# Performance work log

Measured on AMD Instinct MI355X. Metric: run time of the kernel, lower is better.

## Reference

```python
import jax, jax.numpy as jnp
import numpy as np

B, CIN, COUT, K, SDIM, H, W = 8, 512, 256, 3, 512, 64, 64


def _blur_kernel():
    k = jnp.array([1.0, 3.0, 3.0, 1.0], dtype=jnp.float32)
    k = k[None, :] * k[:, None]
    k = k / k.sum()
    return k * 4.0  # upsample_factor ** 2


def setup_inputs() -> dict:
    key = jax.random.key(0)
    ks = jax.random.split(key, 4)
    return {
        "x": jax.random.normal(ks[0], (B, CIN, H, W), jnp.float32),
        "style": jax.random.normal(ks[1], (B, SDIM), jnp.float32),
        "weight": jax.random.normal(ks[2], (1, COUT, CIN, K, K), jnp.float32),
        "mod_weight": jax.random.normal(ks[3], (CIN, SDIM), jnp.float32),
        "mod_bias": jnp.ones((CIN,), jnp.float32),
    }


def reference(x, style, weight, mod_weight, mod_bias):
    b, cin, h, w = x.shape
    cout = weight.shape[1]
    k = weight.shape[-1]
    scale = 1.0 / np.sqrt(cin * k * k)          # fan_in of conv weight
    mod_scale = 1.0 / np.sqrt(mod_weight.shape[1])  # EqualLinear scale

    # modulation: EqualLinear(style) -> [B, Cin]
    s = style @ (mod_weight * mod_scale).T + mod_bias

    # per-sample modulated + demodulated weight [B, Cout, Cin, K, K]
    wmod = scale * weight * s[:, None, :, None, None]
    demod = jax.lax.rsqrt(jnp.sum(wmod * wmod, axis=(2, 3, 4)) + 1e-8)
    wmod = wmod * demod[:, :, None, None, None]

    # conv_transpose2d(stride=2, padding=0) == dilated conv with lhs_dilation=2,
    # padding K-1 on each side, spatially flipped kernel. Output (H-1)*2 + K.
    wflip = jnp.flip(wmod, axis=(-2, -1))

    def per_sample(xi, wi):
        return jax.lax.conv_general_dilated(
            xi[None], wi, window_strides=(1, 1),
            padding=[(k - 1, k - 1)] * 2, lhs_dilation=(2, 2),
            dimension_numbers=("NCHW", "OIHW", "NCHW"))[0]

    out = jax.vmap(per_sample)(x, wflip)  # [B, Cout, 2H+1, 2W+1] for K=3

    # Blur (upfirdn2d, up=1): torch does conv2d with flip(kernel);
    # lax conv is also correlation, so use flipped kernel, depthwise.
    bk = jnp.flip(_blur_kernel(), (0, 1))
    p = 4 - 2 - (k - 1)
    pad0 = (p + 1) // 2 + 1
    pad1 = p // 2 + 1
    wblur = jnp.broadcast_to(bk[None, None], (cout, 1, 4, 4))
    out = jax.lax.conv_general_dilated(
        out, wblur, (1, 1), [(pad0, pad1), (pad0, pad1)],
        feature_group_count=cout,
        dimension_numbers=("NCHW", "OIHW", "NCHW"))
    return out  # [B, Cout, 2H, 2W]
```

## Files before the change

### kernel.cpp

```cpp
#include <hip/hip_runtime.h>
#include <hip/hip_bf16.h>
#include <stdint.h>

typedef unsigned short u16;
typedef __attribute__((ext_vector_type(8))) short short8;
typedef __attribute__((ext_vector_type(4))) float floatx4;

__device__ __forceinline__ u16 f2bf(float f) {
    union { unsigned int i; float f; } v; v.f = f;
    unsigned int r = v.i + 0x7fff + ((v.i >> 16) & 1);
    return (u16)(r >> 16);
}

#define OFF_S    0
#define OFF_DEM  16384
#define OFF_W2   32768
#define OFF_BM   1048576
#define OFF_XMT  16777216

__global__ void k_style(const float* __restrict__ style, const float* __restrict__ mw,
                        const float* __restrict__ mb, float* __restrict__ S) {
    int t = blockIdx.x * 256 + threadIdx.x;
    int b = t >> 9, ci = t & 511;
    const float* sr = style + b * 512;
    const float* wr = mw + ci * 512;
    float acc = 0.f;
    for (int d = 0; d < 512; d += 4) {
        float4 sv = *(const float4*)(sr + d);
        float4 wv = *(const float4*)(wr + d);
        acc += sv.x * wv.x + sv.y * wv.y + sv.z * wv.z + sv.w * wv.w;
    }
    S[t] = acc * 0.044194173824159216f + mb[ci];
}

__global__ void k_w2(const float* __restrict__ w, float* __restrict__ W2) {
    int t = blockIdx.x * 256 + threadIdx.x;
    const float* p = w + t * 9;
    float a = 0.f;
    #pragma unroll
    for (int i = 0; i < 9; ++i) { float v = p[i]; a += v * v; }
    W2[t] = a;
}

__global__ void k_demod(const float* __restrict__ W2, const float* __restrict__ S,
                        float* __restrict__ D) {
    int t = blockIdx.x * 256 + threadIdx.x;
    int b = t >> 8, co = t & 255;
    const float* wr = W2 + co * 512;
    const float* sr = S + b * 512;
    float a = 0.f;
    for (int ci = 0; ci < 512; ++ci) { float s = sr[ci]; a += wr[ci] * s * s; }
    D[t] = 0.014731391274719738f * rsqrtf(a * (1.0f / 4608.0f) + 1e-8f);
}

__global__ void k_bmat(const float* __restrict__ Wt, u16* __restrict__ Bm) {
    int t = blockIdx.x * 256 + threadIdx.x;
    int ci = t & 511;
    int rest = t >> 9;
    int co = rest & 255;
    int p = rest >> 8;
    int py = p >> 1, px = p & 1;
    const float KT[2][3][3] = {
        {{0.f,1.f,3.f},{3.f,3.f,1.f},{1.f,0.f,0.f}},
        {{0.f,0.f,1.f},{1.f,3.f,3.f},{3.f,1.f,0.f}}
    };
    float wv[3][3];
    const float* wp = Wt + (co * 512 + ci) * 9;
    #pragma unroll
    for (int a = 0; a < 3; ++a)
        #pragma unroll
        for (int bq = 0; bq < 3; ++bq) wv[a][bq] = wp[a * 3 + bq];
    int n = py * 512 + co * 2 + px;
    size_t base = (size_t)n * 4608 + ci;
    #pragma unroll
    for (int dyi = 0; dyi < 3; ++dyi) {
        #pragma unroll
        for (int dxi = 0; dxi < 3; ++dxi) {
            float val = 0.f;
            #pragma unroll
            for (int a = 0; a < 3; ++a) {
                float ky = KT[py][dyi][a];
                #pragma unroll
                for (int bq = 0; bq < 3; ++bq)
                    val += wv[a][bq] * (ky * KT[px][dxi][bq]);
            }
            Bm[base + (dyi * 3 + dxi) * 512] = f2bf(val * 0.0625f);
        }
    }
}

__global__ void k_zero(u16* __restrict__ XMT) {
    size_t t = (size_t)blockIdx.x * 256 + threadIdx.x;
    *(short8*)(XMT + t * 8) = (short8)0;
}

__global__ void k_fill(const float* __restrict__ X, const float* __restrict__ S,
                       u16* __restrict__ XMT) {
    __shared__ __align__(16) u16 tile[64][80];
    int blk = blockIdx.x;
    int ci0g = (blk & 7) * 64;
    int h = (blk >> 3) & 63;
    int b = blk >> 9;
    int t = threadIdx.x;
    #pragma unroll
    for (int it = 0; it < 4; ++it) {
        int idx = it * 256 + t;
        int ci_l = idx >> 4, ch = idx & 15;
        float4 v = *(const float4*)(X + (((b * 512 + ci0g + ci_l) * 64 + h) * 64 + ch * 4));
        float s = S[b * 512 + ci0g + ci_l];
        tile[ch * 4 + 0][ci_l] = f2bf(v.x * s);
        tile[ch * 4 + 1][ci_l] = f2bf(v.y * s);
        tile[ch * 4 + 2][ci_l] = f2bf(v.z * s);
        tile[ch * 4 + 3][ci_l] = f2bf(v.w * s);
    }
    __syncthreads();
    #pragma unroll
    for (int it = 0; it < 2; ++it) {
        int idx = it * 256 + t;
        int wl = idx >> 3, c8 = idx & 7;
        short8 v = *(const short8*)(&tile[wl][c8 * 8]);
        *(short8*)(XMT + (((size_t)(b * 66 + h + 1) * 66 + (wl + 1)) * 512 + ci0g + c8 * 8)) = v;
    }
}


#define GLDS(SRC, DST) __builtin_amdgcn_global_load_lds( \
    (const __attribute__((address_space(1))) void*)(SRC), \
    (__attribute__((address_space(3))) void*)(DST), 16, 0, 0)

#define BAR() do { asm volatile("" ::: "memory"); \
                   __builtin_amdgcn_s_barrier(); \
                   asm volatile("" ::: "memory"); } while (0)

#define WAITV(n) asm volatile("s_waitcnt vmcnt(" #n ")" ::: "memory")

#define STAGE_A(d, h, kt) do { int _o = offA(kt); \
    GLDS(X  + preA[h][0] + _o, smem + (d)*32768 + (h)*16384 + t*16); \
    GLDS(X  + preA[h][1] + _o, smem + (d)*32768 + (h)*16384 + 8192 + t*16); \
  } while (0)
#define STAGE_B(d, h, kt) do { int _o = (kt)*64; \
    GLDS(Bm + preB[h][0] + _o, smem + 65536 + (d)*32768 + (h)*16384 + t*16); \
    GLDS(Bm + preB[h][1] + _o, smem + 65536 + (d)*32768 + (h)*16384 + 8192 + t*16); \
  } while (0)

#define LOAD_A(d, mh) do { \
    _Pragma("unroll") \
    for (int mt_ = 0; mt_ < 4; ++mt_) { \
      afr[mt_][0] = *(const short8*)(smem + (d)*32768 + (mh)*16384 + mt_*2048 + baseMA + cb0); \
      afr[mt_][1] = *(const short8*)(smem + (d)*32768 + (mh)*16384 + mt_*2048 + baseMA + cb1); \
    } } while (0)
#define LOAD_B(d, nh, DST) do { \
    _Pragma("unroll") \
    for (int nt_ = 0; nt_ < 2; ++nt_) { \
      DST[nt_][0] = *(const short8*)(smem + 65536 + (d)*32768 + (nh)*16384 + nt_*2048 + baseNB + cb0); \
      DST[nt_][1] = *(const short8*)(smem + 65536 + (d)*32768 + (nh)*16384 + nt_*2048 + baseNB + cb1); \
    } } while (0)

#define MMA(mh, nh, BF) do { \
    __builtin_amdgcn_s_setprio(1); \
    _Pragma("unroll") \
    for (int mt_ = 0; mt_ < 4; ++mt_) \
      _Pragma("unroll") \
      for (int nt_ = 0; nt_ < 2; ++nt_) { \
        acc[mh][mt_][nh][nt_] = __builtin_amdgcn_mfma_f32_16x16x32_bf16( \
            afr[mt_][0], BF[nt_][0], acc[mh][mt_][nh][nt_], 0, 0, 0); \
        acc[mh][mt_][nh][nt_] = __builtin_amdgcn_mfma_f32_16x16x32_bf16( \
            afr[mt_][1], BF[nt_][1], acc[mh][mt_][nh][nt_], 0, 0, 0); \
      } \
    __builtin_amdgcn_s_setprio(0); \
  } while (0)

__global__ __launch_bounds__(512, 2)
void k_main8(const u16* __restrict__ X, const u16* __restrict__ Bm,
             const float* __restrict__ D, float* __restrict__ out) {
    __shared__ __align__(16) char smem[131072];
    const int t = threadIdx.x;
    const int swz = (blockIdx.x & 7) * 64 + (blockIdx.x >> 3);
    const int bn = swz & 3, bm = swz >> 2;
    const int w = t >> 6, L = t & 63;
    const int wm = w >> 2, wn = w & 3;
    const int quad = L >> 4, col = L & 15;

    int preA[2][2], preB[2][2];
    #pragma unroll
    for (int h = 0; h < 2; ++h)
      #pragma unroll
      for (int i = 0; i < 2; ++i) {
        int sig = i * 512 + t;
        int ml = sig >> 3;
        int ks = (sig & 7) ^ (ml & 7);
        int mg = bm * 256 + h * 128 + ml;
        int b_ = mg >> 12, r = (mg >> 6) & 63, c = mg & 63;
        preA[h][i] = ((b_ * 66 + r) * 66 + c) * 512 + ks * 8;
        int ng = bn * 256 + h * 128 + ml;
        preB[h][i] = ng * 4608 + ks * 8;
      }
    auto offA = [](int kt) {
        int j = kt >> 3;
        int dy = (j * 11) >> 5;
        int dx = j - dy * 3;
        return (dy * 66 + dx) * 512 + (kt & 7) * 64;
    };

    const int baseMA = (wm * 64 + col) * 128;
    const int baseNB = (wn * 32 + col) * 128;
    const int cb0 = ((0 * 4 + quad) ^ (col & 7)) * 16;
    const int cb1 = ((1 * 4 + quad) ^ (col & 7)) * 16;

    short8 afr[4][2], bf0[2][2], bf1[2][2];
    floatx4 acc[2][4][2][2];
    #pragma unroll
    for (int mh = 0; mh < 2; ++mh)
      #pragma unroll
      for (int mt = 0; mt < 4; ++mt)
        #pragma unroll
        for (int nh = 0; nh < 2; ++nh)
          #pragma unroll
          for (int nt = 0; nt < 2; ++nt)
            acc[mh][mt][nh][nt] = (floatx4){0.f, 0.f, 0.f, 0.f};

    STAGE_A(0, 0, 0); STAGE_B(0, 0, 0);
    STAGE_A(0, 1, 0); STAGE_B(0, 1, 0);
    STAGE_A(1, 0, 1); STAGE_B(1, 0, 1);
    WAITV(4);
    BAR();

    #pragma unroll 1
    for (int it = 0; it < 35; ++it) {
        const int k = 2 * it;
        LOAD_A(0, 0); LOAD_B(0, 0, bf0);
        STAGE_A(1, 1, k + 1);
        BAR(); MMA(0, 0, bf0); BAR();
        LOAD_B(0, 1, bf1);
        STAGE_B(1, 1, k + 1);
        BAR(); MMA(0, 1, bf1); BAR();
        LOAD_A(0, 1);
        STAGE_A(0, 0, k + 2);
        BAR(); MMA(1, 0, bf0); BAR();
        STAGE_B(0, 0, k + 2);
        WAITV(4);
        BAR(); MMA(1, 1, bf1); BAR();
        LOAD_A(1, 0); LOAD_B(1, 0, bf0);
        STAGE_A(0, 1, k + 2);
        BAR(); MMA(0, 0, bf0); BAR();
        LOAD_B(1, 1, bf1);
        STAGE_B(0, 1, k + 2);
        BAR(); MMA(0, 1, bf1); BAR();
        LOAD_A(1, 1);
        STAGE_A(1, 0, k + 3);
        BAR(); MMA(1, 0, bf0); BAR();
        STAGE_B(1, 0, k + 3);
        WAITV(4);
        BAR(); MMA(1, 1, bf1); BAR();
    }

    LOAD_A(0, 0); LOAD_B(0, 0, bf0);
    STAGE_A(1, 1, 71);
    BAR(); MMA(0, 0, bf0); BAR();
    LOAD_B(0, 1, bf1);
    STAGE_B(1, 1, 71);
    BAR(); MMA(0, 1, bf1); BAR();
    LOAD_A(0, 1);
    BAR(); MMA(1, 0, bf0); BAR();
    WAITV(0);
    BAR(); MMA(1, 1, bf1); BAR();
    LOAD_A(1, 0); LOAD_B(1, 0, bf0);
    BAR(); MMA(0, 0, bf0); BAR();
    LOAD_B(1, 1, bf1);
    BAR(); MMA(0, 1, bf1); BAR();
    LOAD_A(1, 1);
    BAR(); MMA(1, 0, bf0); BAR();
    BAR(); MMA(1, 1, bf1); BAR();

    const int b   = bm >> 4;
    const int r0  = (bm & 15) * 4;
    const int py  = bn >> 1;
    const int co0 = (bn & 1) * 128;
    float dvals[2][2];
    #pragma unroll
    for (int nh = 0; nh < 2; ++nh)
      #pragma unroll
      for (int nt = 0; nt < 2; ++nt)
        dvals[nh][nt] = D[b * 256 + co0 + nh * 64 + wn * 16 + nt * 8 + (col >> 1)];

    float* ep = (float*)smem;
    #pragma unroll
    for (int rl = 0; rl < 4; ++rl) {
        if (wm == (rl & 1)) {
            const int mh = rl >> 1;
            #pragma unroll
            for (int nh = 0; nh < 2; ++nh)
              #pragma unroll
              for (int nt = 0; nt < 2; ++nt) {
                float dsv = dvals[nh][nt];
                int coL = nh * 64 + wn * 16 + nt * 8 + (col >> 1);
                #pragma unroll
                for (int mt = 0; mt < 4; ++mt)
                  #pragma unroll
                  for (int reg = 0; reg < 4; ++reg) {
                    int x = 2 * (mt * 16 + quad * 4 + reg) + (col & 1);
                    ep[coL * 132 + x] = acc[mh][mt][nh][nt][reg] * dsv;
                  }
              }
        }
        __syncthreads();
        #pragma unroll
        for (int itc = 0; itc < 8; ++itc) {
            int s = itc * 512 + t;
            int co = s >> 5, xi = s & 31;
            float4 v = *(const float4*)(ep + co * 132 + xi * 4);
            size_t o = ((size_t)((b * 256 + co0 + co) * 128 + (2 * (r0 + rl) + py))) * 128 + xi * 4;
            *(float4*)(out + o) = v;
        }
        __syncthreads();
    }
}

extern "C" void kernel_launch(void* const* d_in, const int* in_sizes, int n_in,
                              void* d_out, int out_size, void* d_ws, size_t ws_size,
                              hipStream_t stream) {
    const float* x      = (const float*)d_in[0];
    const float* style  = (const float*)d_in[1];
    const float* weight = (const float*)d_in[2];
    const float* mw     = (const float*)d_in[3];
    const float* mb     = (const float*)d_in[4];
    float* out = (float*)d_out;
    char* ws = (char*)d_ws;
    float* S   = (float*)(ws + OFF_S);
    float* DEM = (float*)(ws + OFF_DEM);
    float* W2  = (float*)(ws + OFF_W2);
    u16*  BM   = (u16*)(ws + OFF_BM);
    u16*  XMT  = (u16*)(ws + OFF_XMT);

    k_style<<<16,   256, 0, stream>>>(style, mw, mb, S);
    k_w2   <<<512,  256, 0, stream>>>(weight, W2);
    k_demod<<<8,    256, 0, stream>>>(W2, S, DEM);
    k_bmat <<<2048, 256, 0, stream>>>(weight, BM);
    k_zero <<<8712, 256, 0, stream>>>(XMT);
    k_fill <<<4096, 256, 0, stream>>>(x, S, XMT);
    k_main8<<<512,  512, 0, stream>>>(XMT, BM, DEM, out);
}
```

Before: 476.7 us.

## Parallelize prologue kernels, fold border zeroing into fill, swizzle fill LDS

The style and demodulation reductions now give each output one wavefront and reduce with shuffles, so they launch many more blocks instead of a handful of serial-loop threads. The weight-to-B-matrix kernel stages each block's weights through shared memory so the strided 9-float reads become coalesced. The separate zeroing pass over the padded activation buffer is removed and only the one-pixel halo is zeroed inside the fill kernel. The fill kernel's transpose tile gets an XOR swizzle to cut LDS bank conflicts. The risk is that halo zeroing is now spread across fill blocks, and correctness depends on every border cell being covered.

Measured after the change: 428.4 us. 1.11x faster.

```diff
diff --git a/kernel.cpp b/kernel.cpp
--- a/kernel.cpp
+++ b/kernel.cpp
@@ -20,17 +20,20 @@
 
 __global__ void k_style(const float* __restrict__ style, const float* __restrict__ mw,
                         const float* __restrict__ mb, float* __restrict__ S) {
-    int t = blockIdx.x * 256 + threadIdx.x;
-    int b = t >> 9, ci = t & 511;
-    const float* sr = style + b * 512;
-    const float* wr = mw + ci * 512;
-    float acc = 0.f;
-    for (int d = 0; d < 512; d += 4) {
-        float4 sv = *(const float4*)(sr + d);
-        float4 wv = *(const float4*)(wr + d);
-        acc += sv.x * wv.x + sv.y * wv.y + sv.z * wv.z + sv.w * wv.w;
-    }
-    S[t] = acc * 0.044194173824159216f + mb[ci];
+    int g = blockIdx.x * 4 + (threadIdx.x >> 6);
+    int lane = threadIdx.x & 63;
+    int b = g >> 9, ci = g & 511;
+    const float* sr = style + b * 512 + lane * 8;
+    const float* wr = mw + ci * 512 + lane * 8;
+    float4 s0 = *(const float4*)(sr);
+    float4 s1 = *(const float4*)(sr + 4);
+    float4 w0 = *(const float4*)(wr);
+    float4 w1 = *(const float4*)(wr + 4);
+    float acc = s0.x * w0.x + s0.y * w0.y + s0.z * w0.z + s0.w * w0.w
+              + s1.x * w1.x + s1.y * w1.y + s1.z * w1.z + s1.w * w1.w;
+    #pragma unroll
+    for (int o = 32; o; o >>= 1) acc += __shfl_xor(acc, o, 64);
+    if (lane == 0) S[g] = acc * 0.044194173824159216f + mb[ci];
 }
 
 __global__ void k_w2(const float* __restrict__ w, float* __restrict__ W2) {
@@ -44,32 +47,44 @@
 
 __global__ void k_demod(const float* __restrict__ W2, const float* __restrict__ S,
                         float* __restrict__ D) {
-    int t = blockIdx.x * 256 + threadIdx.x;
-    int b = t >> 8, co = t & 255;
-    const float* wr = W2 + co * 512;
-    const float* sr = S + b * 512;
-    float a = 0.f;
-    for (int ci = 0; ci < 512; ++ci) { float s = sr[ci]; a += wr[ci] * s * s; }
-    D[t] = 0.014731391274719738f * rsqrtf(a * (1.0f / 4608.0f) + 1e-8f);
+    int g = blockIdx.x * 4 + (threadIdx.x >> 6);
+    int lane = threadIdx.x & 63;
+    int b = g >> 8, co = g & 255;
+    const float* wr = W2 + co * 512 + lane * 8;
+    const float* sr = S + b * 512 + lane * 8;
+    float4 w0 = *(const float4*)(wr);
+    float4 w1 = *(const float4*)(wr + 4);
+    float4 s0 = *(const float4*)(sr);
+    float4 s1 = *(const float4*)(sr + 4);
+    float a = w0.x * s0.x * s0.x + w0.y * s0.y * s0.y + w0.z * s0.z * s0.z + w0.w * s0.w * s0.w
+            + w1.x * s1.x * s1.x + w1.y * s1.y * s1.y + w1.z * s1.z * s1.z + w1.w * s1.w * s1.w;
+    #pragma unroll
+    for (int o = 32; o; o >>= 1) a += __shfl_xor(a, o, 64);
+    if (lane == 0) D[g] = 0.014731391274719738f * rsqrtf(a * (1.0f / 4608.0f) + 1e-8f);
 }
 
 __global__ void k_bmat(const float* __restrict__ Wt, u16* __restrict__ Bm) {
-    int t = blockIdx.x * 256 + threadIdx.x;
-    int ci = t & 511;
-    int rest = t >> 9;
-    int co = rest & 255;
-    int p = rest >> 8;
+    __shared__ float wl[2304];
+    int blk = blockIdx.x;
+    int tid = threadIdx.x;
+    int ci0 = (blk & 1) * 256;
+    int co  = (blk >> 1) & 255;
+    int p   = blk >> 9;
     int py = p >> 1, px = p & 1;
+    int wbase = co * 4608 + ci0 * 9;
+    #pragma unroll
+    for (int j = 0; j < 9; ++j) wl[j * 256 + tid] = Wt[wbase + j * 256 + tid];
+    __syncthreads();
     const float KT[2][3][3] = {
         {{0.f,1.f,3.f},{3.f,3.f,1.f},{1.f,0.f,0.f}},
         {{0.f,0.f,1.f},{1.f,3.f,3.f},{3.f,1.f,0.f}}
     };
     float wv[3][3];
-    const float* wp = Wt + (co * 512 + ci) * 9;
     #pragma unroll
     for (int a = 0; a < 3; ++a)
         #pragma unroll
-        for (int bq = 0; bq < 3; ++bq) wv[a][bq] = wp[a * 3 + bq];
+        for (int bq = 0; bq < 3; ++bq) wv[a][bq] = wl[tid * 9 + a * 3 + bq];
+    int ci = ci0 + tid;
     int n = py * 512 + co * 2 + px;
     size_t base = (size_t)n * 4608 + ci;
     #pragma unroll
@@ -89,11 +104,6 @@
     }
 }
 
-__global__ void k_zero(u16* __restrict__ XMT) {
-    size_t t = (size_t)blockIdx.x * 256 + threadIdx.x;
-    *(short8*)(XMT + t * 8) = (short8)0;
-}
-
 __global__ void k_fill(const float* __restrict__ X, const float* __restrict__ S,
                        u16* __restrict__ XMT) {
     __shared__ __align__(16) u16 tile[64][80];
@@ -102,23 +112,36 @@
     int h = (blk >> 3) & 63;
     int b = blk >> 9;
     int t = threadIdx.x;
+    if (t < 16) {
+        int x = (t >> 3) ? 65 : 0;
+        int c8 = t & 7;
+        *(short8*)(XMT + ((size_t)(b * 66 + h + 1) * 66 + x) * 512 + ci0g + c8 * 8) = (short8)0;
+    }
+    if (h == 0 || h == 63) {
+        int y = (h == 0) ? 0 : 65;
+        for (int s0 = t; s0 < 528; s0 += 256) {
+            int x = s0 >> 3, c8 = s0 & 7;
+            *(short8*)(XMT + ((size_t)(b * 66 + y) * 66 + x) * 512 + ci0g + c8 * 8) = (short8)0;
+        }
+    }
     #pragma unroll
     for (int it = 0; it < 4; ++it) {
         int idx = it * 256 + t;
         int ci_l = idx >> 4, ch = idx & 15;
         float4 v = *(const float4*)(X + (((b * 512 + ci0g + ci_l) * 64 + h) * 64 + ch * 4));
         float s = S[b * 512 + ci0g + ci_l];
-        tile[ch * 4 + 0][ci_l] = f2bf(v.x * s);
-        tile[ch * 4 + 1][ci_l] = f2bf(v.y * s);
-        tile[ch * 4 + 2][ci_l] = f2bf(v.z * s);
-        tile[ch * 4 + 3][ci_l] = f2bf(v.w * s);
+        int cisw = ci_l ^ ((ch & 7) << 3);
+        tile[ch * 4 + 0][cisw] = f2bf(v.x * s);
+        tile[ch * 4 + 1][cisw] = f2bf(v.y * s);
+        tile[ch * 4 + 2][cisw] = f2bf(v.z * s);
+        tile[ch * 4 + 3][cisw] = f2bf(v.w * s);
     }
     __syncthreads();
     #pragma unroll
     for (int it = 0; it < 2; ++it) {
         int idx = it * 256 + t;
         int wl = idx >> 3, c8 = idx & 7;
-        short8 v = *(const short8*)(&tile[wl][c8 * 8]);
+        short8 v = *(const short8*)(&tile[wl][(c8 ^ ((wl >> 2) & 7)) * 8]);
         *(short8*)(XMT + (((size_t)(b * 66 + h + 1) * 66 + (wl + 1)) * 512 + ci0g + c8 * 8)) = v;
     }
 }
@@ -332,11 +355,10 @@
     u16*  BM   = (u16*)(ws + OFF_BM);
     u16*  XMT  = (u16*)(ws + OFF_XMT);
 
-    k_style<<<16,   256, 0, stream>>>(style, mw, mb, S);
+    k_style<<<1024, 256, 0, stream>>>(style, mw, mb, S);
     k_w2   <<<512,  256, 0, stream>>>(weight, W2);
-    k_demod<<<8,    256, 0, stream>>>(W2, S, DEM);
+    k_demod<<<512,  256, 0, stream>>>(W2, S, DEM);
     k_bmat <<<2048, 256, 0, stream>>>(weight, BM);
-    k_zero <<<8712, 256, 0, stream>>>(XMT);
     k_fill <<<4096, 256, 0, stream>>>(x, S, XMT);
     k_main8<<<512,  512, 0, stream>>>(XMT, BM, DEM, out);
 }
```
